# Kernel tuning notes

Measured on AMD Instinct MI355X. Metric: run time of the kernel, lower is better.

## Reference

```python
import jax, jax.numpy as jnp
import numpy as np

NUM_NODES = 16384
NUM_EDGES = 131072
NUM_MOLS = 512
H = 256          # hidden_dim
L = 3            # num_hidden_layers
NUM_RBF = 50
CUTOFF = 5.0
IN_DIM = 5
D_IN = IN_DIM + 3  # atom_types + spherical coords


def setup_inputs() -> dict:
    ks = jax.random.split(jax.random.key(0), 32)
    n = lambda k, s: jax.random.normal(k, s, dtype=jnp.float32) * 0.05
    return {
        "atom_types": jax.random.uniform(ks[0], (NUM_NODES, IN_DIM), dtype=jnp.float32),
        "coords_spherical": jax.random.normal(ks[1], (NUM_NODES, 3), dtype=jnp.float32),
        "edge_dist": jax.random.uniform(ks[2], (NUM_EDGES,), dtype=jnp.float32) * CUTOFF,
        "edge_index": jax.random.randint(ks[3], (2, NUM_EDGES), 0, NUM_NODES, dtype=jnp.int32),
        "node2mol": jnp.arange(NUM_NODES, dtype=jnp.int32) // (NUM_NODES // NUM_MOLS),
        "emb_Wm": n(ks[4], (D_IN, H)), "emb_bm": jnp.zeros((H,), jnp.float32),
        "emb_Wp": n(ks[5], (D_IN, H)), "emb_bp": jnp.zeros((H,), jnp.float32),
        "attn_Wqm": n(ks[6], (L, H, H)), "attn_Wkm": n(ks[7], (L, H, H)), "attn_Wvm": n(ks[8], (L, H, H)),
        "attn_Wqp": n(ks[9], (L, H, H)), "attn_Wkp": n(ks[10], (L, H, H)), "attn_Wvp": n(ks[11], (L, H, H)),
        "attn_We": n(ks[12], (L, NUM_RBF)), "attn_be": jnp.zeros((L,), jnp.float32),
        "mp_We": n(ks[13], (L, NUM_RBF, H)), "mp_be": jnp.zeros((L, H), jnp.float32),
        "mp_Wm": n(ks[14], (L, H, H)), "mp_bm": jnp.zeros((L, H), jnp.float32),
        "mp_Wp": n(ks[15], (L, H, H)), "mp_bp": jnp.zeros((L, H), jnp.float32),
        "ln_g": jnp.ones((L, H), jnp.float32), "ln_b": jnp.zeros((L, H), jnp.float32),
        "proj_W": n(ks[16], (H, H)), "proj_b": jnp.zeros((H,), jnp.float32),
        "head_W1": n(ks[17], (2 * H, H)), "head_b1": jnp.zeros((H,), jnp.float32),
        "head_W2": n(ks[18], (H, H // 2)), "head_b2": jnp.zeros((H // 2,), jnp.float32),
        "head_W3": n(ks[19], (H // 2, 1)), "head_b3": jnp.zeros((1,), jnp.float32),
    }


def _seg_softmax(s, seg, n):
    m = jax.ops.segment_max(s, seg, num_segments=n)
    e = jnp.exp(s - m[seg])
    z = jax.ops.segment_sum(e, seg, num_segments=n)
    return e / (z[seg] + 1e-9)


def _layernorm(x, g, b):
    mu = x.mean(-1, keepdims=True)
    v = ((x - mu) ** 2).mean(-1, keepdims=True)
    return (x - mu) * jax.lax.rsqrt(v + 1e-5) * g + b


def _forward(atom_types, coords_spherical, edge_dist,
             emb_Wm, emb_bm, emb_Wp, emb_bp,
             attn_Wqm, attn_Wkm, attn_Wvm, attn_Wqp, attn_Wkp, attn_Wvp, attn_We, attn_be,
             mp_We, mp_be, mp_Wm, mp_bm, mp_Wp, mp_bp,
             ln_g, ln_b, proj_W, proj_b,
             head_W1, head_b1, head_W2, head_b2, head_W3, head_b3,
             edge_index, node2mol):
    src, dst = edge_index[0], edge_index[1]
    N = NUM_NODES

    # --- RBF expansion (Schutt 2018): 50 gaussians on [0, cutoff] * cosine cutoff ---
    centers = jnp.linspace(0.0, CUTOFF, NUM_RBF)
    delta = CUTOFF / NUM_RBF
    env = 0.5 * (jnp.cos(jnp.pi * edge_dist / CUTOFF) + 1.0) * (edge_dist < CUTOFF)
    rbf = jnp.exp(-0.5 * ((edge_dist[:, None] - centers) / delta) ** 2) * env[:, None]  # [E, R]

    # --- Complex polar embedding ---
    x = jnp.concatenate([atom_types, coords_spherical], axis=-1)  # [N, 8]
    mag = jax.nn.softplus(x @ emb_Wm + emb_bm)
    ph = jnp.pi * jnp.tanh(x @ emb_Wp + emb_bp)

    for l in range(L):
        # --- Complex polar attention: |q||k| cos(phi_q - phi_k), edge bias from rbf ---
        qm, km, vm = mag @ attn_Wqm[l], mag @ attn_Wkm[l], mag @ attn_Wvm[l]
        qp, kp, vp = ph @ attn_Wqp[l], ph @ attn_Wkp[l], ph @ attn_Wvp[l]
        score = jnp.sum(qm[dst] * km[src] * jnp.cos(qp[dst] - kp[src]), axis=-1) / jnp.sqrt(float(H))
        score = score + rbf @ attn_We[l] + attn_be[l]          # [E]
        alpha = _seg_softmax(score, dst, N)                    # [E]
        new_mag = jax.ops.segment_sum(alpha[:, None] * vm[src], dst, num_segments=N)
        new_ph = jax.ops.segment_sum(alpha[:, None] * vp[src], dst, num_segments=N)

        # --- Complex message passing gated by RBF profile ---
        gate = jax.nn.silu(rbf @ mp_We[l] + mp_be[l])          # [E, H]
        agg_m = jax.ops.segment_sum(gate * new_mag[src], dst, num_segments=N)
        agg_p = jax.ops.segment_sum(gate * new_ph[src], dst, num_segments=N)
        new_mag = new_mag + agg_m @ mp_Wm[l] + mp_bm[l]
        new_ph = new_ph + agg_p @ mp_Wp[l] + mp_bp[l]

        # --- residual + LayerNorm on magnitude (dropout = identity at eval) ---
        new_mag = new_mag + mag
        new_ph = new_ph + ph
        mag = _layernorm(new_mag, ln_g[l], ln_b[l])
        ph = new_ph

    # --- real projection + dual (mean, sum) pooling per molecule ---
    atom_repr = (mag * jnp.cos(ph)) @ proj_W + proj_b          # [N, H]
    s = jax.ops.segment_sum(atom_repr, node2mol, num_segments=NUM_MOLS)
    cnt = jax.ops.segment_sum(jnp.ones((N, 1), atom_repr.dtype), node2mol, num_segments=NUM_MOLS)
    mol = jnp.concatenate([s / jnp.maximum(cnt, 1.0), s], axis=-1)  # [B, 2H]

    h = jax.nn.silu(mol @ head_W1 + head_b1)
    h = jax.nn.silu(h @ head_W2 + head_b2)
    return h @ head_W3 + head_b3                               # [B, 1]


def reference(atom_types, coords_spherical, edge_dist,
              emb_Wm, emb_bm, emb_Wp, emb_bp,
              attn_Wqm, attn_Wkm, attn_Wvm, attn_Wqp, attn_Wkp, attn_Wvp, attn_We, attn_be,
              mp_We, mp_be, mp_Wm, mp_bm, mp_Wp, mp_bp,
              ln_g, ln_b, proj_W, proj_b,
              head_W1, head_b1, head_W2, head_b2, head_W3, head_b3,
              edge_index, node2mol):
    return _forward(atom_types, coords_spherical, edge_dist,
                    emb_Wm, emb_bm, emb_Wp, emb_bp,
                    attn_Wqm, attn_Wkm, attn_Wvm, attn_Wqp, attn_Wkp, attn_Wvp, attn_We, attn_be,
                    mp_We, mp_be, mp_Wm, mp_bm, mp_Wp, mp_bp,
                    ln_g, ln_b, proj_W, proj_b,
                    head_W1, head_b1, head_W2, head_b2, head_W3, head_b3,
                    edge_index, node2mol)
```

## Files before the change

kernel.cpp:

```cpp
#include <hip/hip_runtime.h>
#include <math.h>

#define N_NODES 16384
#define N_EDGES 131072
#define N_MOLS 512
#define HDIM 256
#define NLAYER 3
#define NRBF 50
#define CUT 5.0f
#define HH (HDIM*HDIM)

typedef unsigned short u16;
typedef __attribute__((ext_vector_type(8))) short short8v;
typedef __attribute__((ext_vector_type(4))) float f32x4;
typedef __attribute__((ext_vector_type(4))) unsigned short u16x4;
typedef __attribute__((ext_vector_type(8))) unsigned short u16x8;
typedef __attribute__((ext_vector_type(2))) unsigned short u16x2;

__device__ __forceinline__ float softplusf(float x){ return fmaxf(x,0.f)+log1pf(expf(-fabsf(x))); }
__device__ __forceinline__ float siluf(float x){ return x/(1.f+expf(-x)); }
__device__ __forceinline__ float bf2f(u16 u){ union{unsigned int i; float f;}v; v.i=((unsigned int)u)<<16; return v.f; }
__device__ __forceinline__ u16 f2bf(float f){ union{float f; unsigned int i;}v; v.f=f; unsigned int r = v.i + 0x7FFFu + ((v.i>>16)&1u); return (u16)(r>>16); }

__device__ __forceinline__ void gload_lds16(const void* g, void* l){
  __builtin_amdgcn_global_load_lds((const __attribute__((address_space(1))) unsigned int*)g,
                                   (__attribute__((address_space(3))) unsigned int*)l, 16, 0, 0);
}

__global__ void k_hist(const int* __restrict__ dst, int* __restrict__ cnt){
  int e = blockIdx.x*256 + threadIdx.x;
  if(e < N_EDGES) atomicAdd(&cnt[dst[e]], 1);
}

__global__ __launch_bounds__(1024) void k_scan(const int* __restrict__ cnt,
                                               int* __restrict__ rowptr,
                                               int* __restrict__ cursor){
  __shared__ int part[1024];
  int tid = threadIdx.x;
  int base = tid*16;
  int loc[16]; int s=0;
  #pragma unroll
  for(int i=0;i<16;i++){ loc[i]=s; s+=cnt[base+i]; }
  part[tid]=s; __syncthreads();
  for(int off=1; off<1024; off<<=1){
    int v = (tid>=off)? part[tid-off] : 0;
    __syncthreads();
    part[tid] += v;
    __syncthreads();
  }
  int pre = (tid==0)?0:part[tid-1];
  #pragma unroll
  for(int i=0;i<16;i++){ int v = pre+loc[i]; rowptr[base+i]=v; cursor[base+i]=v; }
  if(tid==1023) rowptr[N_NODES]=part[1023];
}

__global__ void k_scatter(const int* __restrict__ dst, int* __restrict__ cursor,
                          int* __restrict__ perm){
  int e = blockIdx.x*256+threadIdx.x;
  if(e<N_EDGES){ int p = atomicAdd(&cursor[dst[e]],1); perm[p]=e; }
}

__global__ void k_rbf(const float* __restrict__ dist, u16* __restrict__ rbf){
  int gid = blockIdx.x*256+threadIdx.x;
  int e = gid>>6, r = gid&63;
  u16 o = 0;
  if(r<NRBF){
    float d = dist[e];
    float env = 0.5f*(cosf(3.14159265358979f*d/CUT)+1.f) * (d<CUT ? 1.f:0.f);
    float c = CUT*(float)r/(float)(NRBF-1);
    float u = (d - c)/(CUT/(float)NRBF);
    o = f2bf(expf(-0.5f*u*u)*env);
  }
  rbf[(size_t)e*64+r] = o;
}

struct WDesc { const float* src; u16* dst; int K; int dK; };
struct WArgs { WDesc d[28]; };
__global__ __launch_bounds__(256) void k_wconv(WArgs a){
  WDesc w = a.d[blockIdx.x];
  int t = blockIdx.y;
  int ky = t >> 3, nx = t & 7;
  if(ky*32 >= w.dK) return;
  __shared__ float tile[32][33];
  int tid = threadIdx.x;
  int kk = tid >> 3, n4 = (tid & 7)*4;
  int k = ky*32 + kk;
  float4 v = {0.f,0.f,0.f,0.f};
  if(k < w.K) v = *(const float4*)(w.src + (size_t)k*HDIM + nx*32 + n4);
  tile[kk][n4+0]=v.x; tile[kk][n4+1]=v.y; tile[kk][n4+2]=v.z; tile[kk][n4+3]=v.w;
  __syncthreads();
  int nn = tid >> 3, k4 = (tid & 7)*4;
  u16x4 o;
  #pragma unroll
  for(int j=0;j<4;j++) o[j] = f2bf(tile[k4+j][nn]);
  *(u16x4*)(w.dst + (size_t)(nx*32+nn)*w.dK + ky*32 + k4) = o;
}

__global__ void k_embed(const float* __restrict__ at, const float* __restrict__ co,
                        const float* __restrict__ Wm, const float* __restrict__ bm,
                        const float* __restrict__ Wp, const float* __restrict__ bp,
                        float* __restrict__ mag, float* __restrict__ ph,
                        u16* __restrict__ magb, u16* __restrict__ phb){
  int n = blockIdx.x; int h = threadIdx.x;
  __shared__ float x[8];
  if(threadIdx.x<5) x[threadIdx.x] = at[n*5+threadIdx.x];
  else if(threadIdx.x<8) x[threadIdx.x] = co[n*3+threadIdx.x-5];
  __syncthreads();
  float tm=bm[h], tp=bp[h];
  #pragma unroll
  for(int i=0;i<8;i++){ tm = fmaf(x[i],Wm[i*HDIM+h],tm); tp = fmaf(x[i],Wp[i*HDIM+h],tp); }
  size_t idx = (size_t)n*HDIM+h;
  float m = softplusf(tm);
  float p = 3.14159265358979f*tanhf(tp);
  mag[idx]=m; ph[idx]=p; magb[idx]=f2bf(m); phb[idx]=f2bf(p);
}

template<int MODE>
__device__ __forceinline__ void gemm_body(const u16* __restrict__ A,
                                          const u16* __restrict__ Bt,
                                          const float* __restrict__ bias,
                                          void* __restrict__ outp, int K, int ostr){
  __shared__ __align__(16) u16 As[128*64];
  __shared__ __align__(16) u16 Bs[64*64];
  int tid = threadIdx.x;
  int lane = tid & 63, wid = tid >> 6;
  int wm = wid & 1, wn = wid >> 1;
  int m0 = blockIdx.y * 128;
  int n0 = blockIdx.x * 64;
  const size_t Kb = (size_t)K*2;
  f32x4 acc[4][2] = {};
  for(int k0=0; k0<K; k0+=64){
    #pragma unroll
    for(int it=0; it<4; it++){
      int off = it*4096 + tid*16;
      int row = off >> 7, col = off & 127;
      const char* g = (const char*)A + (size_t)(m0+row)*Kb + (size_t)k0*2 + col;
      gload_lds16(g, (char*)As + it*4096 + wid*1024);
    }
    #pragma unroll
    for(int it=0; it<2; it++){
      int off = it*4096 + tid*16;
      int row = off >> 7, col = off & 127;
      const char* g = (const char*)Bt + (size_t)(n0+row)*Kb + (size_t)k0*2 + col;
      gload_lds16(g, (char*)Bs + it*4096 + wid*1024);
    }
    __syncthreads();
    #pragma unroll
    for(int ks=0; ks<2; ks++){
      int kl = ks*32 + (lane>>4)*8;
      short8v a[4], b[2];
      #pragma unroll
      for(int fm=0; fm<4; fm++){
        int m = wm*64 + fm*16 + (lane&15);
        a[fm] = *(const short8v*)&As[m*64 + kl];
      }
      #pragma unroll
      for(int fn=0; fn<2; fn++){
        int n = wn*32 + fn*16 + (lane&15);
        b[fn] = *(const short8v*)&Bs[n*64 + kl];
      }
      #pragma unroll
      for(int fm=0; fm<4; fm++)
        #pragma unroll
        for(int fn=0; fn<2; fn++)
          acc[fm][fn] = __builtin_amdgcn_mfma_f32_16x16x32_bf16(a[fm], b[fn], acc[fm][fn], 0,0,0);
    }
    __syncthreads();
  }
  int ro = (lane>>4)*4, co = lane&15;
  #pragma unroll
  for(int fm=0; fm<4; fm++){
    #pragma unroll
    for(int fn=0; fn<2; fn++){
      int col = n0 + wn*32 + fn*16 + co;
      float bv = (MODE!=0) ? bias[col] : 0.f;
      #pragma unroll
      for(int r=0; r<4; r++){
        int row = m0 + wm*64 + fm*16 + ro + r;
        float v = acc[fm][fn][r] + bv;
        size_t ci = (size_t)row*ostr + col;
        if(MODE==0) ((u16*)outp)[ci] = f2bf(v);
        else if(MODE==1) ((u16*)outp)[ci] = f2bf(siluf(v));
        else if(MODE==2) ((float*)outp)[ci] += v;
        else ((float*)outp)[ci] = v;
      }
    }
  }
}

struct QkvArgs { const u16* Wt[6]; u16* out[6]; };
__global__ __launch_bounds__(256,2) void k_gemm_qkv(const u16* __restrict__ magb,
                                                    const u16* __restrict__ phb, QkvArgs q){
  int z = blockIdx.z;
  const u16* A = (z<3) ? magb : phb;
  gemm_body<0>(A, q.Wt[z], nullptr, q.out[z], HDIM, 1536);
}
__global__ __launch_bounds__(256,2) void k_gemm_gate(const u16* __restrict__ rbfb,
                                                     const u16* __restrict__ Wt,
                                                     const float* __restrict__ be,
                                                     u16* __restrict__ gate){
  gemm_body<1>(rbfb, Wt, be, gate, 64, 256);
}
struct MpArgs { const u16* A[2]; const u16* Wt[2]; const float* b[2]; float* C[2]; };
__global__ __launch_bounds__(256,2) void k_gemm_mp(MpArgs a){
  int z = blockIdx.z;
  gemm_body<2>(a.A[z], a.Wt[z], a.b[z], a.C[z], HDIM, 256);
}
__global__ __launch_bounds__(256,2) void k_gemm_proj(const u16* __restrict__ Ab,
                                                     const u16* __restrict__ Wt,
                                                     const float* __restrict__ b,
                                                     float* __restrict__ C){
  gemm_body<3>(Ab, Wt, b, C, HDIM, 256);
}

__global__ __launch_bounds__(256) void k_attn_fused(
    const int* __restrict__ rowptr, const int* __restrict__ perm,
    const int* __restrict__ src,
    const u16* __restrict__ pack, const u16* __restrict__ rbf,
    const float* __restrict__ We, const float* __restrict__ be,
    float* __restrict__ nmag, float* __restrict__ nph,
    u16* __restrict__ npack)
{
  int wid = threadIdx.x >> 6, lane = threadIdx.x & 63;
  int hid = lane >> 5, l = lane & 31;
  int d = blockIdx.x*4 + wid;
  int b = rowptr[d], e = rowptr[d+1];
  const u16* qb = pack + (size_t)d*1536 + l*8;
  u16x8 qm8 = *(const u16x8*)qb;
  u16x8 qp8 = *(const u16x8*)(qb + 256);
  float qmf[8], qpf[8];
  #pragma unroll
  for(int j=0;j<8;j++){ qmf[j]=bf2f(qm8[j]); qpf[j]=bf2f(qp8[j]); }
  float We0 = (2*l   < NRBF) ? We[2*l]   : 0.f;
  float We1 = (2*l+1 < NRBF) ? We[2*l+1] : 0.f;
  float be0 = be[0];
  float z = 0.f;
  float avm[8] = {0,0,0,0,0,0,0,0}, avp[8] = {0,0,0,0,0,0,0,0};
  for(int i = b + hid; i < e; i += 2){
    int ed = perm[i]; int s = src[ed];
    const u16* kb = pack + (size_t)s*1536 + l*8;
    u16x8 km8 = *(const u16x8*)(kb + 512);
    u16x8 kp8 = *(const u16x8*)(kb + 768);
    u16x8 vm8 = *(const u16x8*)(kb + 1024);
    u16x8 vp8 = *(const u16x8*)(kb + 1280);
    u16x2 rb2 = *(const u16x2*)(rbf + (size_t)ed*64 + 2*l);
    float p = 0.f;
    #pragma unroll
    for(int j=0;j<8;j++)
      p = fmaf(qmf[j]*bf2f(km8[j]), __cosf(qpf[j]-bf2f(kp8[j])), p);
    float t = fmaf(bf2f(rb2[0]), We0, fmaf(bf2f(rb2[1]), We1, p*0.0625f));
    #pragma unroll
    for(int off=16; off; off>>=1) t += __shfl_xor(t, off, 64);
    float w = __expf(t + be0);
    z += w;
    #pragma unroll
    for(int j=0;j<8;j++){
      avm[j] = fmaf(w, bf2f(vm8[j]), avm[j]);
      avp[j] = fmaf(w, bf2f(vp8[j]), avp[j]);
    }
  }
  z += __shfl_xor(z, 32, 64);
  #pragma unroll
  for(int j=0;j<8;j++){
    avm[j] += __shfl_xor(avm[j], 32, 64);
    avp[j] += __shfl_xor(avp[j], 32, 64);
  }
  if(hid==0){
    float inv = 1.f/(z + 1e-9f);
    u16x8 mb, pb;
    #pragma unroll
    for(int j=0;j<8;j++){ avm[j]*=inv; avp[j]*=inv; mb[j]=f2bf(avm[j]); pb[j]=f2bf(avp[j]); }
    size_t no = (size_t)d*256 + l*8;
    *(float4*)(nmag + no)     = make_float4(avm[0],avm[1],avm[2],avm[3]);
    *(float4*)(nmag + no + 4) = make_float4(avm[4],avm[5],avm[6],avm[7]);
    *(float4*)(nph + no)      = make_float4(avp[0],avp[1],avp[2],avp[3]);
    *(float4*)(nph + no + 4)  = make_float4(avp[4],avp[5],avp[6],avp[7]);
    u16* nb = npack + (size_t)d*512 + l*8;
    *(u16x8*)nb = mb;
    *(u16x8*)(nb + 256) = pb;
  }
}

__global__ __launch_bounds__(256) void k_mp_agg(const int* __restrict__ rowptr, const int* __restrict__ perm,
                         const int* __restrict__ src, const u16* __restrict__ gate,
                         const u16* __restrict__ npack,
                         u16* __restrict__ aggm, u16* __restrict__ aggp){
  int wid = threadIdx.x >> 6, lane = threadIdx.x & 63;
  int hid = lane >> 5, l = lane & 31;
  int n = blockIdx.x*4 + wid;
  int b = rowptr[n], e = rowptr[n+1];
  float am[8] = {0,0,0,0,0,0,0,0}, ap[8] = {0,0,0,0,0,0,0,0};
  for(int i = b + hid; i < e; i += 2){
    int ed = perm[i]; int s = src[ed];
    u16x8 g8 = *(const u16x8*)(gate + (size_t)ed*256 + l*8);
    const u16* nb = npack + (size_t)s*512 + l*8;
    u16x8 m8 = *(const u16x8*)nb;
    u16x8 p8 = *(const u16x8*)(nb + 256);
    #pragma unroll
    for(int j=0;j<8;j++){
      float g = bf2f(g8[j]);
      am[j] = fmaf(g, bf2f(m8[j]), am[j]);
      ap[j] = fmaf(g, bf2f(p8[j]), ap[j]);
    }
  }
  #pragma unroll
  for(int j=0;j<8;j++){
    am[j] += __shfl_xor(am[j], 32, 64);
    ap[j] += __shfl_xor(ap[j], 32, 64);
  }
  if(hid==0){
    u16x8 amb, apb;
    #pragma unroll
    for(int j=0;j<8;j++){ amb[j]=f2bf(am[j]); apb[j]=f2bf(ap[j]); }
    size_t o = (size_t)n*256 + l*8;
    *(u16x8*)(aggm + o) = amb;
    *(u16x8*)(aggp + o) = apb;
  }
}

template<int LAST>
__global__ __launch_bounds__(256) void k_resid_ln(const float* __restrict__ nmag, const float* __restrict__ nph,
                           float* __restrict__ mag, float* __restrict__ ph,
                           u16* __restrict__ magb, u16* __restrict__ phb,
                           u16* __restrict__ tcosb,
                           const float* __restrict__ g, const float* __restrict__ b){
  int n = blockIdx.x, tid = threadIdx.x;
  size_t idx = (size_t)n*HDIM+tid;
  float t = nmag[idx] + mag[idx];
  float s1=t, s2=t*t;
  #pragma unroll
  for(int off=32; off; off>>=1){ s1 += __shfl_down(s1,off,64); s2 += __shfl_down(s2,off,64); }
  __shared__ float w1[4], w2[4], bc[2];
  int wid = tid>>6, lane = tid&63;
  if(lane==0){ w1[wid]=s1; w2[wid]=s2; }
  __syncthreads();
  if(tid==0){
    float a=w1[0]+w1[1]+w1[2]+w1[3];
    float q=w2[0]+w2[1]+w2[2]+w2[3];
    float mu = a*(1.f/HDIM);
    float var = q*(1.f/HDIM) - mu*mu;
    bc[0]=mu; bc[1]=rsqrtf(var+1e-5f);
  }
  __syncthreads();
  float mu=bc[0], rs=bc[1];
  float ln = (t-mu)*rs*g[tid]+b[tid];
  float p2 = nph[idx] + ph[idx];
  if(LAST){
    tcosb[idx] = f2bf(ln*__cosf(p2));
  } else {
    mag[idx] = ln; magb[idx] = f2bf(ln);
    ph[idx] = p2; phb[idx] = f2bf(p2);
  }
}

__global__ void k_pool(const float* __restrict__ arepr, const int* __restrict__ n2m,
                       float* __restrict__ spool, float* __restrict__ cntf){
  int gid = blockIdx.x*256+threadIdx.x;
  int n = gid>>8, h = gid&255;
  int m = n2m[n];
  atomicAdd(&spool[(size_t)m*HDIM+h], arepr[(size_t)n*HDIM+h]);
  if(h==0) atomicAdd(&cntf[m], 1.f);
}

__global__ __launch_bounds__(256) void k_head(const float* __restrict__ spool, const float* __restrict__ cntf,
                       const float* __restrict__ W1, const float* __restrict__ b1,
                       const float* __restrict__ W2, const float* __restrict__ b2,
                       const float* __restrict__ W3, const float* __restrict__ b3,
                       float* __restrict__ out){
  __shared__ float smol[2*HDIM];
  __shared__ float sh1[HDIM];
  __shared__ float sh2[HDIM/2];
  int m = blockIdx.x, tid = threadIdx.x;
  float sv = spool[(size_t)m*HDIM+tid];
  float c = cntf[m];
  smol[tid] = sv/fmaxf(c,1.f);
  smol[HDIM+tid] = sv;
  __syncthreads();
  float a = b1[tid];
  for(int i=0;i<2*HDIM;i++) a = fmaf(smol[i], W1[i*HDIM+tid], a);
  sh1[tid] = siluf(a);
  __syncthreads();
  if(tid<128){
    float a2 = b2[tid];
    for(int i=0;i<HDIM;i++) a2 = fmaf(sh1[i], W2[i*128+tid], a2);
    sh2[tid] = siluf(a2);
  }
  __syncthreads();
  if(tid<64){
    float p = sh2[tid]*W3[tid] + sh2[tid+64]*W3[tid+64];
    #pragma unroll
    for(int off=32; off; off>>=1) p += __shfl_down(p,off,64);
    if(tid==0) out[m] = p + b3[0];
  }
}

extern "C" void kernel_launch(void* const* d_in, const int* in_sizes, int n_in,
                              void* d_out, int out_size, void* d_ws, size_t ws_size,
                              hipStream_t stream){
  const float* atom_types = (const float*)d_in[0];
  const float* coords     = (const float*)d_in[1];
  const float* edge_dist  = (const float*)d_in[2];
  const int*   edge_index = (const int*)d_in[3];
  const int*   node2mol   = (const int*)d_in[4];
  const float* emb_Wm = (const float*)d_in[5];
  const float* emb_bm = (const float*)d_in[6];
  const float* emb_Wp = (const float*)d_in[7];
  const float* emb_bp = (const float*)d_in[8];
  const float* attn_Wqm = (const float*)d_in[9];
  const float* attn_Wkm = (const float*)d_in[10];
  const float* attn_Wvm = (const float*)d_in[11];
  const float* attn_Wqp = (const float*)d_in[12];
  const float* attn_Wkp = (const float*)d_in[13];
  const float* attn_Wvp = (const float*)d_in[14];
  const float* attn_We  = (const float*)d_in[15];
  const float* attn_be  = (const float*)d_in[16];
  const float* mp_We = (const float*)d_in[17];
  const float* mp_be = (const float*)d_in[18];
  const float* mp_Wm = (const float*)d_in[19];
  const float* mp_bm = (const float*)d_in[20];
  const float* mp_Wp = (const float*)d_in[21];
  const float* mp_bp = (const float*)d_in[22];
  const float* ln_g = (const float*)d_in[23];
  const float* ln_b = (const float*)d_in[24];
  const float* proj_W = (const float*)d_in[25];
  const float* proj_b = (const float*)d_in[26];
  const float* head_W1 = (const float*)d_in[27];
  const float* head_b1 = (const float*)d_in[28];
  const float* head_W2 = (const float*)d_in[29];
  const float* head_b2 = (const float*)d_in[30];
  const float* head_W3 = (const float*)d_in[31];
  const float* head_b3 = (const float*)d_in[32];
  float* out = (float*)d_out;

  float* ws = (float*)d_ws;
  const size_t NH = (size_t)N_NODES*HDIM;
  size_t o = 0;
  float* mag = ws + o; o += NH;
  float* ph  = ws + o; o += NH;
  float* nmag= ws + o; o += NH;
  float* nph = ws + o; o += NH;
  float* spool = ws + o; o += (size_t)N_MOLS*HDIM;
  float* cntf  = ws + o; o += N_MOLS;
  int* rowptr = (int*)(ws + o); o += N_NODES+1;
  int* cnt    = (int*)(ws + o); o += N_NODES;
  int* cursor = (int*)(ws + o); o += N_NODES;
  int* perm   = (int*)(ws + o); o += N_EDGES + 1;
  u16* magb = (u16*)(ws + o); o += NH/2;
  u16* phb  = (u16*)(ws + o); o += NH/2;
  u16* aggmb= (u16*)(ws + o); o += NH/2;
  u16* aggpb= (u16*)(ws + o); o += NH/2;
  u16* npack= (u16*)(ws + o); o += NH;
  u16* rbfb = (u16*)(ws + o); o += (size_t)N_EDGES*32;
  u16* arena= (u16*)(ws + o); o += (size_t)N_EDGES*128;
  u16* wt   = (u16*)(ws + o); o += (25*(size_t)HH + 3*HDIM*64)/2;
  u16* pack = arena;
  u16* gateb = arena;
  float* arepr = nmag;
  u16* tcosb = aggmb;

  const int* src = edge_index;
  const int* dst = edge_index + N_EDGES;

  WArgs wa;
  for(int l=0;l<NLAYER;l++){
    const float* srcs[6] = {attn_Wqm+(size_t)l*HH, attn_Wkm+(size_t)l*HH, attn_Wvm+(size_t)l*HH,
                            attn_Wqp+(size_t)l*HH, attn_Wkp+(size_t)l*HH, attn_Wvp+(size_t)l*HH};
    for(int j=0;j<6;j++){ wa.d[l*6+j] = { srcs[j], wt + (size_t)(l*6+j)*HH, HDIM, HDIM }; }
    wa.d[18+l] = { mp_Wm+(size_t)l*HH, wt + (size_t)(18+l)*HH, HDIM, HDIM };
    wa.d[21+l] = { mp_Wp+(size_t)l*HH, wt + (size_t)(21+l)*HH, HDIM, HDIM };
    wa.d[25+l] = { mp_We+(size_t)l*NRBF*HDIM, wt + (size_t)25*HH + (size_t)l*HDIM*64, NRBF, 64 };
  }
  wa.d[24] = { proj_W, wt + (size_t)24*HH, HDIM, HDIM };

  hipMemsetAsync(cnt, 0, N_NODES*sizeof(int), stream);
  k_hist<<<N_EDGES/256,256,0,stream>>>(dst, cnt);
  k_scan<<<1,1024,0,stream>>>(cnt, rowptr, cursor);
  k_scatter<<<N_EDGES/256,256,0,stream>>>(dst, cursor, perm);
  k_wconv<<<dim3(28,64),256,0,stream>>>(wa);
  k_rbf<<<(N_EDGES*64)/256,256,0,stream>>>(edge_dist, rbfb);
  k_embed<<<N_NODES,256,0,stream>>>(atom_types, coords, emb_Wm, emb_bm, emb_Wp, emb_bp,
                                    mag, ph, magb, phb);

  dim3 gn(HDIM/64, N_NODES/128);
  dim3 ge(HDIM/64, N_EDGES/128);
  for(int l=0;l<NLAYER;l++){
    QkvArgs qa;
    const int zoff[6] = {0, 512, 1024, 256, 768, 1280};
    for(int j=0;j<6;j++){ qa.Wt[j] = wt + (size_t)(l*6+j)*HH; qa.out[j] = pack + zoff[j]; }
    k_gemm_qkv<<<dim3(4,128,6),256,0,stream>>>(magb, phb, qa);
    k_attn_fused<<<N_NODES/4,256,0,stream>>>(rowptr, perm, src, pack,
                                             rbfb, attn_We+(size_t)l*NRBF, attn_be+l,
                                             nmag, nph, npack);
    k_gemm_gate<<<ge,256,0,stream>>>(rbfb, wt + (size_t)25*HH + (size_t)l*HDIM*64,
                                     mp_be+(size_t)l*HDIM, gateb);
    k_mp_agg<<<N_NODES/4,256,0,stream>>>(rowptr, perm, src, gateb, npack, aggmb, aggpb);
    MpArgs ma;
    ma.A[0]=aggmb; ma.A[1]=aggpb;
    ma.Wt[0]=wt + (size_t)(18+l)*HH; ma.Wt[1]=wt + (size_t)(21+l)*HH;
    ma.b[0]=mp_bm+(size_t)l*HDIM; ma.b[1]=mp_bp+(size_t)l*HDIM;
    ma.C[0]=nmag; ma.C[1]=nph;
    k_gemm_mp<<<dim3(4,128,2),256,0,stream>>>(ma);
    if(l < NLAYER-1)
      k_resid_ln<0><<<N_NODES,256,0,stream>>>(nmag, nph, mag, ph, magb, phb, nullptr,
                                              ln_g+(size_t)l*HDIM, ln_b+(size_t)l*HDIM);
    else
      k_resid_ln<1><<<N_NODES,256,0,stream>>>(nmag, nph, mag, ph, magb, phb, tcosb,
                                              ln_g+(size_t)l*HDIM, ln_b+(size_t)l*HDIM);
  }
  k_gemm_proj<<<gn,256,0,stream>>>(tcosb, wt + (size_t)24*HH, proj_b, arepr);
  hipMemsetAsync(spool, 0, ((size_t)N_MOLS*HDIM+N_MOLS)*sizeof(float), stream);
  k_pool<<<NH/256,256,0,stream>>>(arepr, node2mol, spool, cntf);
  k_head<<<N_MOLS,256,0,stream>>>(spool, cntf, head_W1, head_b1, head_W2, head_b2, head_W3, head_b3, out);
}
```

Before: 943.6 us.

## Precompute sin/cos-rotated Q/K in QKV GEMM and permute edge data to CSR order

The QKV projection is rewritten so each block computes the magnitude and phase GEMMs together and writes m*cos(p) and m*sin(p) for Q and K. The per-edge cos(q_p-k_p) product in attention then becomes two plain dot products by the angle-difference identity. Edge RBF features, source indices and the gate GEMM output are now stored in destination-sorted order, so the gather kernels read them contiguously instead of going through perm. The cost is a few extra sincos calls in the GEMM epilogue and slightly different bf16 rounding of the attention logits.

```diff
diff --git a/kernel.cpp b/kernel.cpp
--- a/kernel.cpp
+++ b/kernel.cpp
@@ -54,15 +54,22 @@
   if(tid==1023) rowptr[N_NODES]=part[1023];
 }
 
-__global__ void k_scatter(const int* __restrict__ dst, int* __restrict__ cursor,
-                          int* __restrict__ perm){
+__global__ void k_scatter(const int* __restrict__ dst, const int* __restrict__ src,
+                          int* __restrict__ cursor,
+                          int* __restrict__ perm, int* __restrict__ srcp){
   int e = blockIdx.x*256+threadIdx.x;
-  if(e<N_EDGES){ int p = atomicAdd(&cursor[dst[e]],1); perm[p]=e; }
-}
-
-__global__ void k_rbf(const float* __restrict__ dist, u16* __restrict__ rbf){
+  if(e<N_EDGES){
+    int p = atomicAdd(&cursor[dst[e]],1);
+    perm[p]=e;
+    srcp[p]=src[e];
+  }
+}
+
+__global__ void k_rbf(const float* __restrict__ dist, const int* __restrict__ perm,
+                      u16* __restrict__ rbfp){
   int gid = blockIdx.x*256+threadIdx.x;
-  int e = gid>>6, r = gid&63;
+  int i = gid>>6, r = gid&63;
+  int e = perm[i];
   u16 o = 0;
   if(r<NRBF){
     float d = dist[e];
@@ -71,7 +78,7 @@
     float u = (d - c)/(CUT/(float)NRBF);
     o = f2bf(expf(-0.5f*u*u)*env);
   }
-  rbf[(size_t)e*64+r] = o;
+  rbfp[(size_t)i*64+r] = o;
 }
 
 struct WDesc { const float* src; u16* dst; int K; int dK; };
@@ -173,14 +180,13 @@
     #pragma unroll
     for(int fn=0; fn<2; fn++){
       int col = n0 + wn*32 + fn*16 + co;
-      float bv = (MODE!=0) ? bias[col] : 0.f;
+      float bv = bias ? bias[col] : 0.f;
       #pragma unroll
       for(int r=0; r<4; r++){
         int row = m0 + wm*64 + fm*16 + ro + r;
         float v = acc[fm][fn][r] + bv;
         size_t ci = (size_t)row*ostr + col;
-        if(MODE==0) ((u16*)outp)[ci] = f2bf(v);
-        else if(MODE==1) ((u16*)outp)[ci] = f2bf(siluf(v));
+        if(MODE==1) ((u16*)outp)[ci] = f2bf(siluf(v));
         else if(MODE==2) ((float*)outp)[ci] += v;
         else ((float*)outp)[ci] = v;
       }
@@ -188,18 +194,101 @@
   }
 }
 
-struct QkvArgs { const u16* Wt[6]; u16* out[6]; };
-__global__ __launch_bounds__(256,2) void k_gemm_qkv(const u16* __restrict__ magb,
-                                                    const u16* __restrict__ phb, QkvArgs q){
+struct Qkv2Args { const u16* Wm[3]; const u16* Wp[3]; u16* qpk; u16* kvpk; };
+__global__ __launch_bounds__(256,2) void k_gemm_qkv2(const u16* __restrict__ magb,
+                                                     const u16* __restrict__ phb,
+                                                     Qkv2Args a){
+  __shared__ __align__(16) u16 Am[128*64];
+  __shared__ __align__(16) u16 Ap[128*64];
+  __shared__ __align__(16) u16 Bm[64*64];
+  __shared__ __align__(16) u16 Bp[64*64];
   int z = blockIdx.z;
-  const u16* A = (z<3) ? magb : phb;
-  gemm_body<0>(A, q.Wt[z], nullptr, q.out[z], HDIM, 1536);
-}
-__global__ __launch_bounds__(256,2) void k_gemm_gate(const u16* __restrict__ rbfb,
+  const u16* Wmz = a.Wm[z];
+  const u16* Wpz = a.Wp[z];
+  int tid = threadIdx.x;
+  int lane = tid & 63, wid = tid >> 6;
+  int wm = wid & 1, wn = wid >> 1;
+  int m0 = blockIdx.y * 128;
+  int n0 = blockIdx.x * 64;
+  const size_t Kb = 512;
+  f32x4 accm[4][2] = {}, accp[4][2] = {};
+  for(int k0=0; k0<256; k0+=64){
+    #pragma unroll
+    for(int it=0; it<4; it++){
+      int off = it*4096 + tid*16;
+      int row = off >> 7, col = off & 127;
+      size_t go = (size_t)(m0+row)*Kb + (size_t)k0*2 + col;
+      gload_lds16((const char*)magb + go, (char*)Am + it*4096 + wid*1024);
+      gload_lds16((const char*)phb  + go, (char*)Ap + it*4096 + wid*1024);
+    }
+    #pragma unroll
+    for(int it=0; it<2; it++){
+      int off = it*4096 + tid*16;
+      int row = off >> 7, col = off & 127;
+      size_t go = (size_t)(n0+row)*Kb + (size_t)k0*2 + col;
+      gload_lds16((const char*)Wmz + go, (char*)Bm + it*4096 + wid*1024);
+      gload_lds16((const char*)Wpz + go, (char*)Bp + it*4096 + wid*1024);
+    }
+    __syncthreads();
+    #pragma unroll
+    for(int ks=0; ks<2; ks++){
+      int kl = ks*32 + (lane>>4)*8;
+      short8v am[4], ap[4], bm_[2], bp_[2];
+      #pragma unroll
+      for(int fm=0; fm<4; fm++){
+        int m = wm*64 + fm*16 + (lane&15);
+        am[fm] = *(const short8v*)&Am[m*64 + kl];
+        ap[fm] = *(const short8v*)&Ap[m*64 + kl];
+      }
+      #pragma unroll
+      for(int fn=0; fn<2; fn++){
+        int n = wn*32 + fn*16 + (lane&15);
+        bm_[fn] = *(const short8v*)&Bm[n*64 + kl];
+        bp_[fn] = *(const short8v*)&Bp[n*64 + kl];
+      }
+      #pragma unroll
+      for(int fm=0; fm<4; fm++)
+        #pragma unroll
+        for(int fn=0; fn<2; fn++){
+          accm[fm][fn] = __builtin_amdgcn_mfma_f32_16x16x32_bf16(am[fm], bm_[fn], accm[fm][fn], 0,0,0);
+          accp[fm][fn] = __builtin_amdgcn_mfma_f32_16x16x32_bf16(ap[fm], bp_[fn], accp[fm][fn], 0,0,0);
+        }
+    }
+    __syncthreads();
+  }
+  int ro = (lane>>4)*4, co = lane&15;
+  #pragma unroll
+  for(int fm=0; fm<4; fm++){
+    #pragma unroll
+    for(int fn=0; fn<2; fn++){
+      int col = n0 + wn*32 + fn*16 + co;
+      #pragma unroll
+      for(int r=0; r<4; r++){
+        int row = m0 + wm*64 + fm*16 + ro + r;
+        float mv = accm[fm][fn][r];
+        float pv = accp[fm][fn][r];
+        u16 o0, o1;
+        if(z<2){
+          float sn, cs;
+          __sincosf(pv, &sn, &cs);
+          o0 = f2bf(mv*cs); o1 = f2bf(mv*sn);
+        } else {
+          o0 = f2bf(mv); o1 = f2bf(pv);
+        }
+        u16* base = (z==0) ? (a.qpk + (size_t)row*512)
+                           : (a.kvpk + (size_t)row*1024 + (z==2 ? 512 : 0));
+        base[col] = o0;
+        base[col+256] = o1;
+      }
+    }
+  }
+}
+
+__global__ __launch_bounds__(256,2) void k_gemm_gate(const u16* __restrict__ rbfp,
                                                      const u16* __restrict__ Wt,
                                                      const float* __restrict__ be,
                                                      u16* __restrict__ gate){
-  gemm_body<1>(rbfb, Wt, be, gate, 64, 256);
+  gemm_body<1>(rbfp, Wt, be, gate, 64, 256);
 }
 struct MpArgs { const u16* A[2]; const u16* Wt[2]; const float* b[2]; float* C[2]; };
 __global__ __launch_bounds__(256,2) void k_gemm_mp(MpArgs a){
@@ -214,9 +303,9 @@
 }
 
 __global__ __launch_bounds__(256) void k_attn_fused(
-    const int* __restrict__ rowptr, const int* __restrict__ perm,
-    const int* __restrict__ src,
-    const u16* __restrict__ pack, const u16* __restrict__ rbf,
+    const int* __restrict__ rowptr, const int* __restrict__ srcp,
+    const u16* __restrict__ qpack, const u16* __restrict__ kvpack,
+    const u16* __restrict__ rbfp,
     const float* __restrict__ We, const float* __restrict__ be,
     float* __restrict__ nmag, float* __restrict__ nph,
     u16* __restrict__ npack)
@@ -225,29 +314,31 @@
   int hid = lane >> 5, l = lane & 31;
   int d = blockIdx.x*4 + wid;
   int b = rowptr[d], e = rowptr[d+1];
-  const u16* qb = pack + (size_t)d*1536 + l*8;
-  u16x8 qm8 = *(const u16x8*)qb;
-  u16x8 qp8 = *(const u16x8*)(qb + 256);
-  float qmf[8], qpf[8];
-  #pragma unroll
-  for(int j=0;j<8;j++){ qmf[j]=bf2f(qm8[j]); qpf[j]=bf2f(qp8[j]); }
+  const u16* qb = qpack + (size_t)d*512 + l*8;
+  u16x8 qc8 = *(const u16x8*)qb;
+  u16x8 qs8 = *(const u16x8*)(qb + 256);
+  float qcf[8], qsf[8];
+  #pragma unroll
+  for(int j=0;j<8;j++){ qcf[j]=bf2f(qc8[j]); qsf[j]=bf2f(qs8[j]); }
   float We0 = (2*l   < NRBF) ? We[2*l]   : 0.f;
   float We1 = (2*l+1 < NRBF) ? We[2*l+1] : 0.f;
   float be0 = be[0];
   float z = 0.f;
   float avm[8] = {0,0,0,0,0,0,0,0}, avp[8] = {0,0,0,0,0,0,0,0};
   for(int i = b + hid; i < e; i += 2){
-    int ed = perm[i]; int s = src[ed];
-    const u16* kb = pack + (size_t)s*1536 + l*8;
-    u16x8 km8 = *(const u16x8*)(kb + 512);
-    u16x8 kp8 = *(const u16x8*)(kb + 768);
-    u16x8 vm8 = *(const u16x8*)(kb + 1024);
-    u16x8 vp8 = *(const u16x8*)(kb + 1280);
-    u16x2 rb2 = *(const u16x2*)(rbf + (size_t)ed*64 + 2*l);
+    int s = srcp[i];
+    const u16* kb = kvpack + (size_t)s*1024 + l*8;
+    u16x8 kc8 = *(const u16x8*)kb;
+    u16x8 ks8 = *(const u16x8*)(kb + 256);
+    u16x8 vm8 = *(const u16x8*)(kb + 512);
+    u16x8 vp8 = *(const u16x8*)(kb + 768);
+    u16x2 rb2 = *(const u16x2*)(rbfp + (size_t)i*64 + 2*l);
     float p = 0.f;
     #pragma unroll
-    for(int j=0;j<8;j++)
-      p = fmaf(qmf[j]*bf2f(km8[j]), __cosf(qpf[j]-bf2f(kp8[j])), p);
+    for(int j=0;j<8;j++){
+      p = fmaf(qcf[j], bf2f(kc8[j]), p);
+      p = fmaf(qsf[j], bf2f(ks8[j]), p);
+    }
     float t = fmaf(bf2f(rb2[0]), We0, fmaf(bf2f(rb2[1]), We1, p*0.0625f));
     #pragma unroll
     for(int off=16; off; off>>=1) t += __shfl_xor(t, off, 64);
@@ -281,8 +372,8 @@
   }
 }
 
-__global__ __launch_bounds__(256) void k_mp_agg(const int* __restrict__ rowptr, const int* __restrict__ perm,
-                         const int* __restrict__ src, const u16* __restrict__ gate,
+__global__ __launch_bounds__(256) void k_mp_agg(const int* __restrict__ rowptr,
+                         const int* __restrict__ srcp, const u16* __restrict__ gate,
                          const u16* __restrict__ npack,
                          u16* __restrict__ aggm, u16* __restrict__ aggp){
   int wid = threadIdx.x >> 6, lane = threadIdx.x & 63;
@@ -291,8 +382,8 @@
   int b = rowptr[n], e = rowptr[n+1];
   float am[8] = {0,0,0,0,0,0,0,0}, ap[8] = {0,0,0,0,0,0,0,0};
   for(int i = b + hid; i < e; i += 2){
-    int ed = perm[i]; int s = src[ed];
-    u16x8 g8 = *(const u16x8*)(gate + (size_t)ed*256 + l*8);
+    int s = srcp[i];
+    u16x8 g8 = *(const u16x8*)(gate + (size_t)i*256 + l*8);
     const u16* nb = npack + (size_t)s*512 + l*8;
     u16x8 m8 = *(const u16x8*)nb;
     u16x8 p8 = *(const u16x8*)(nb + 256);
@@ -444,17 +535,19 @@
   int* rowptr = (int*)(ws + o); o += N_NODES+1;
   int* cnt    = (int*)(ws + o); o += N_NODES;
   int* cursor = (int*)(ws + o); o += N_NODES;
-  int* perm   = (int*)(ws + o); o += N_EDGES + 1;
+  int* perm   = (int*)(ws + o); o += N_EDGES;
+  int* srcp   = (int*)(ws + o); o += N_EDGES + 1;
   u16* magb = (u16*)(ws + o); o += NH/2;
   u16* phb  = (u16*)(ws + o); o += NH/2;
   u16* aggmb= (u16*)(ws + o); o += NH/2;
   u16* aggpb= (u16*)(ws + o); o += NH/2;
   u16* npack= (u16*)(ws + o); o += NH;
-  u16* rbfb = (u16*)(ws + o); o += (size_t)N_EDGES*32;
-  u16* arena= (u16*)(ws + o); o += (size_t)N_EDGES*128;
+  u16* rbfp = (u16*)(ws + o); o += (size_t)N_EDGES*32;
+  u16* qpack= (u16*)(ws + o); o += NH;
+  u16* kvpack=(u16*)(ws + o); o += 2*NH;
+  o += NH;
   u16* wt   = (u16*)(ws + o); o += (25*(size_t)HH + 3*HDIM*64)/2;
-  u16* pack = arena;
-  u16* gateb = arena;
+  u16* gatep = qpack;
   float* arepr = nmag;
   u16* tcosb = aggmb;
 
@@ -475,25 +568,30 @@
   hipMemsetAsync(cnt, 0, N_NODES*sizeof(int), stream);
   k_hist<<<N_EDGES/256,256,0,stream>>>(dst, cnt);
   k_scan<<<1,1024,0,stream>>>(cnt, rowptr, cursor);
-  k_scatter<<<N_EDGES/256,256,0,stream>>>(dst, cursor, perm);
+  k_scatter<<<N_EDGES/256,256,0,stream>>>(dst, src, cursor, perm, srcp);
   k_wconv<<<dim3(28,64),256,0,stream>>>(wa);
-  k_rbf<<<(N_EDGES*64)/256,256,0,stream>>>(edge_dist, rbfb);
+  k_rbf<<<(N_EDGES*64)/256,256,0,stream>>>(edge_dist, perm, rbfp);
   k_embed<<<N_NODES,256,0,stream>>>(atom_types, coords, emb_Wm, emb_bm, emb_Wp, emb_bp,
                                     mag, ph, magb, phb);
 
   dim3 gn(HDIM/64, N_NODES/128);
   dim3 ge(HDIM/64, N_EDGES/128);
   for(int l=0;l<NLAYER;l++){
-    QkvArgs qa;
-    const int zoff[6] = {0, 512, 1024, 256, 768, 1280};
-    for(int j=0;j<6;j++){ qa.Wt[j] = wt + (size_t)(l*6+j)*HH; qa.out[j] = pack + zoff[j]; }
-    k_gemm_qkv<<<dim3(4,128,6),256,0,stream>>>(magb, phb, qa);
-    k_attn_fused<<<N_NODES/4,256,0,stream>>>(rowptr, perm, src, pack,
-                                             rbfb, attn_We+(size_t)l*NRBF, attn_be+l,
+    Qkv2Args qa;
+    qa.Wm[0] = wt + (size_t)(l*6+0)*HH;
+    qa.Wm[1] = wt + (size_t)(l*6+1)*HH;
+    qa.Wm[2] = wt + (size_t)(l*6+2)*HH;
+    qa.Wp[0] = wt + (size_t)(l*6+3)*HH;
+    qa.Wp[1] = wt + (size_t)(l*6+4)*HH;
+    qa.Wp[2] = wt + (size_t)(l*6+5)*HH;
+    qa.qpk = qpack; qa.kvpk = kvpack;
+    k_gemm_qkv2<<<dim3(4,128,3),256,0,stream>>>(magb, phb, qa);
+    k_attn_fused<<<N_NODES/4,256,0,stream>>>(rowptr, srcp, qpack, kvpack,
+                                             rbfp, attn_We+(size_t)l*NRBF, attn_be+l,
                                              nmag, nph, npack);
-    k_gemm_gate<<<ge,256,0,stream>>>(rbfb, wt + (size_t)25*HH + (size_t)l*HDIM*64,
-                                     mp_be+(size_t)l*HDIM, gateb);
-    k_mp_agg<<<N_NODES/4,256,0,stream>>>(rowptr, perm, src, gateb, npack, aggmb, aggpb);
+    k_gemm_gate<<<ge,256,0,stream>>>(rbfp, wt + (size_t)25*HH + (size_t)l*HDIM*64,
+                                     mp_be+(size_t)l*HDIM, gatep);
+    k_mp_agg<<<N_NODES/4,256,0,stream>>>(rowptr, srcp, gatep, npack, aggmb, aggpb);
     MpArgs ma;
     ma.A[0]=aggmb; ma.A[1]=aggpb;
     ma.Wt[0]=wt + (size_t)(18+l)*HH; ma.Wt[1]=wt + (size_t)(21+l)*HH;
```

Result: no change. 956.1 us (+1.3%).
